# Kernel tuning notes

Measured on AMD Instinct MI355X. Metric: run time of the kernel, lower is better.

Reference implementation:

```python
import jax, jax.numpy as jnp
import numpy as np

B, G, K, KD = 16384, 17, 12, 16      # batch, games, kicks/game, kick feature dim
DK, DM, H, T = 16, 32, 2, 4          # d_kick, d_model, n_attn_heads, n_targets
SD, H1, H2, HH = 64, 256, 128, 32    # static_dim, backbone hidden dims, head hidden
AO = H * DM                          # attention output dim = 64
EPS = 1e-5
NEG_INF = float('-inf')


def setup_inputs() -> dict:
    ks = jax.random.split(jax.random.key(0), 18)
    n = lambda i, s, sc=0.05: jax.random.normal(ks[i], s, jnp.float32) * sc
    x_static = jax.random.normal(ks[0], (B, SD), jnp.float32)
    x_kicks = jax.random.normal(ks[1], (B, G, K, KD), jnp.float32)
    # masks: True = real game / kick; force position 0 valid so no row is fully padded
    outer_mask = jax.random.bernoulli(ks[2], 0.9, (B, G)).at[:, 0].set(True)
    inner_mask = jax.random.bernoulli(ks[3], 0.85, (B, G, K)).at[:, :, 0].set(True)
    return dict(
        x_static=x_static, x_kicks=x_kicks,
        W_ke=n(4, (KD, DK)), b_ke=jnp.zeros((DK,), jnp.float32),
        q_inner=n(5, (1, DK), 0.02),
        W_ge=n(6, (DK, DM)), b_ge=jnp.zeros((DM,), jnp.float32),
        pos_emb=n(7, (G, DM), 0.02),
        q_outer=n(8, (T * H, DM), 0.02),
        log_temp=jnp.zeros((T,), jnp.float32),
        ln_g=jnp.ones((T, AO), jnp.float32), ln_b=jnp.zeros((T, AO), jnp.float32),
        W1=n(9, (SD, H1)), b1=jnp.zeros((H1,), jnp.float32),
        g1=jnp.ones((H1,), jnp.float32), be1=jnp.zeros((H1,), jnp.float32),
        m1=n(10, (H1,)), v1=jax.random.uniform(ks[11], (H1,), jnp.float32) + 0.5,
        W2=n(12, (H1, H2)), b2=jnp.zeros((H2,), jnp.float32),
        g2=jnp.ones((H2,), jnp.float32), be2=jnp.zeros((H2,), jnp.float32),
        m2=n(13, (H2,)), v2=jax.random.uniform(ks[14], (H2,), jnp.float32) + 0.5,
        Wh1=n(15, (T, H2 + AO, HH)), bh1=jnp.zeros((T, HH), jnp.float32),
        Wh2=n(16, (T, HH)), bh2=jnp.zeros((T,), jnp.float32),
        outer_mask=outer_mask, inner_mask=inner_mask)


def _forward(x_static, x_kicks, W_ke, b_ke, q_inner, W_ge, b_ge, pos_emb,
             q_outer, log_temp, ln_g, ln_b, W1, b1, g1, be1, m1, v1,
             W2, b2, g2, be2, m2, v2, Wh1, bh1, Wh2, bh2,
             outer_mask, inner_mask):
    # kick encoder: Linear -> ReLU, [B,G,K,KD] -> [B,G,K,DK]
    kick_enc = jax.nn.relu(jnp.einsum('bgkd,de->bgke', x_kicks, W_ke) + b_ke)
    # inner AttentionPool: single learned query over kicks within each game
    ai = jnp.einsum('d,bgkd->bgk', q_inner[0], kick_enc) * (DK ** -0.5)
    ai = jnp.where(inner_mask, ai, NEG_INF)
    wi = jnp.nan_to_num(jax.nn.softmax(ai, axis=-1))       # all-masked rows -> 0
    per_game = jnp.einsum('bgk,bgkd->bgd', wi, kick_enc)   # [B,G,DK]
    # game encoder + learned positional embedding
    encoded = jax.nn.relu(per_game @ W_ge + b_ge) + pos_emb[None]  # [B,G,DM]
    # outer AttentionPool: T*H learned queries over games, per-target temperature
    ao = jnp.einsum('qd,bgd->bqg', q_outer, encoded) * (DM ** -0.5)
    ao = ao * jnp.repeat(jnp.exp(-log_temp), H)[None, :, None]
    ao = jnp.where(outer_mask[:, None, :], ao, NEG_INF)
    wo = jnp.nan_to_num(jax.nn.softmax(ao, axis=-1))
    pooled = jnp.einsum('bqg,bgd->bqd', wo, encoded).reshape(-1, T, AO)  # [B,T,64]
    # per-target LayerNorm on history vector
    mu = pooled.mean(-1, keepdims=True)
    var = ((pooled - mu) ** 2).mean(-1, keepdims=True)
    hist = (pooled - mu) * jax.lax.rsqrt(var + EPS) * ln_g[None] + ln_b[None]
    # backbone: Linear -> BatchNorm(eval) -> ReLU, x2 (dropout = identity in eval)
    z = jax.nn.relu((x_static @ W1 + b1 - m1) * jax.lax.rsqrt(v1 + EPS) * g1 + be1)
    z = jax.nn.relu((z @ W2 + b2 - m2) * jax.lax.rsqrt(v2 + EPS) * g2 + be2)
    # per-target heads on [shared_static ; history_vec]
    head_in = jnp.concatenate(
        [jnp.broadcast_to(z[:, None, :], (z.shape[0], T, H2)), hist], axis=-1)  # [B,T,192]
    h = jax.nn.relu(jnp.einsum('btd,tdh->bth', head_in, Wh1) + bh1[None])
    out = jnp.einsum('bth,th->bt', h, Wh2) + bh2[None]
    return jnp.maximum(out, 0.0)  # all targets non-negative (clamp, not softplus)


def reference(x_static, x_kicks, W_ke, b_ke, q_inner, W_ge, b_ge, pos_emb,
              q_outer, log_temp, ln_g, ln_b, W1, b1, g1, be1, m1, v1,
              W2, b2, g2, be2, m2, v2, Wh1, bh1, Wh2, bh2,
              outer_mask, inner_mask):
    return _forward(x_static, x_kicks, W_ke, b_ke, q_inner, W_ge, b_ge, pos_emb,
                    q_outer, log_temp, ln_g, ln_b, W1, b1, g1, be1, m1, v1,
                    W2, b2, g2, be2, m2, v2, Wh1, bh1, Wh2, bh2,
                    outer_mask, inner_mask)
```

## Files before the change

### kernel.cpp

```cpp
#include <hip/hip_runtime.h>
#include <math.h>

#define NEGM (-1e30f)

__device__ __forceinline__ float4 ld4(const float* p) { return *(const float4*)p; }
__device__ __forceinline__ void fma4(float4& a, float s, const float4 w) {
    a.x += s * w.x; a.y += s * w.y; a.z += s * w.z; a.w += s * w.w;
}
__device__ __forceinline__ float dot4(const float4 a, const float4 b) {
    return (a.x * b.x + a.y * b.y) + (a.z * b.z + a.w * b.w);
}
__device__ __forceinline__ void upd4(float4& p, float rm, float rw, const float4 a) {
    p.x = p.x * rm + rw * a.x; p.y = p.y * rm + rw * a.y;
    p.z = p.z * rm + rw * a.z; p.w = p.w * rm + rw * a.w;
}

__global__ __launch_bounds__(256) void hist_kernel(
    const float* __restrict__ x_kicks,
    const float* __restrict__ W_ke, const float* __restrict__ b_ke,
    const float* __restrict__ q_inner,
    const float* __restrict__ W_ge, const float* __restrict__ b_ge,
    const float* __restrict__ pos_emb, const float* __restrict__ q_outer,
    const float* __restrict__ log_temp,
    const float* __restrict__ ln_g, const float* __restrict__ ln_b,
    const int* __restrict__ outer_mask, const int* __restrict__ inner_mask,
    float* __restrict__ hist)
{
    __shared__ float s_wke[256];
    __shared__ float s_wge[512];
    __shared__ float s_qout[256];
    __shared__ float s_pg[4][17 * 20];
    __shared__ float s_enc[4][17 * 36];
    __shared__ float s_ao[4][136];

    const int tid  = threadIdx.x;
    const int wid  = tid >> 6;
    const int lane = tid & 63;
    const int b    = blockIdx.x * 4 + wid;

    s_wke[tid] = W_ke[tid];
    s_qout[tid] = q_outer[tid];
    s_wge[tid] = W_ge[tid];
    s_wge[tid + 256] = W_ge[tid + 256];
    __syncthreads();

    float* pg  = s_pg[wid];
    float* enc = s_enc[wid];
    float* ao  = s_ao[wid];

    if (lane < 51) {
        const float* xb = x_kicks + ((size_t)b * 204 + lane * 4) * 16;
        const int4 msk = *(const int4*)(inner_mask + (size_t)b * 204 + lane * 4);

        const float4 qi0 = ld4(q_inner + 0), qi1 = ld4(q_inner + 4);
        const float4 qi2 = ld4(q_inner + 8), qi3 = ld4(q_inner + 12);
        const float4 bk0 = ld4(b_ke + 0), bk1 = ld4(b_ke + 4);
        const float4 bk2 = ld4(b_ke + 8), bk3 = ld4(b_ke + 12);

        float m = NEGM, s = 0.f;
        float4 p0 = {0,0,0,0}, p1 = p0, p2 = p0, p3 = p0;

        #pragma unroll
        for (int pp = 0; pp < 4; ++pp) {
            float xs[16];
            {
                float4 x0 = ld4(xb + pp * 16 + 0), x1 = ld4(xb + pp * 16 + 4);
                float4 x2 = ld4(xb + pp * 16 + 8), x3 = ld4(xb + pp * 16 + 12);
                xs[0]=x0.x; xs[1]=x0.y; xs[2]=x0.z; xs[3]=x0.w;
                xs[4]=x1.x; xs[5]=x1.y; xs[6]=x1.z; xs[7]=x1.w;
                xs[8]=x2.x; xs[9]=x2.y; xs[10]=x2.z; xs[11]=x2.w;
                xs[12]=x3.x; xs[13]=x3.y; xs[14]=x3.z; xs[15]=x3.w;
            }
            float4 a0 = bk0, a1 = bk1, a2 = bk2, a3 = bk3;
            #pragma unroll
            for (int i = 0; i < 16; ++i) {
                float xi = xs[i];
                fma4(a0, xi, *(float4*)&s_wke[i * 16 + 0]);
                fma4(a1, xi, *(float4*)&s_wke[i * 16 + 4]);
                fma4(a2, xi, *(float4*)&s_wke[i * 16 + 8]);
                fma4(a3, xi, *(float4*)&s_wke[i * 16 + 12]);
            }
            a0.x=fmaxf(a0.x,0.f); a0.y=fmaxf(a0.y,0.f); a0.z=fmaxf(a0.z,0.f); a0.w=fmaxf(a0.w,0.f);
            a1.x=fmaxf(a1.x,0.f); a1.y=fmaxf(a1.y,0.f); a1.z=fmaxf(a1.z,0.f); a1.w=fmaxf(a1.w,0.f);
            a2.x=fmaxf(a2.x,0.f); a2.y=fmaxf(a2.y,0.f); a2.z=fmaxf(a2.z,0.f); a2.w=fmaxf(a2.w,0.f);
            a3.x=fmaxf(a3.x,0.f); a3.y=fmaxf(a3.y,0.f); a3.z=fmaxf(a3.z,0.f); a3.w=fmaxf(a3.w,0.f);

            float sc = (dot4(a0, qi0) + dot4(a1, qi1) + dot4(a2, qi2) + dot4(a3, qi3)) * 0.25f;
            int mk = (pp == 0) ? msk.x : (pp == 1) ? msk.y : (pp == 2) ? msk.z : msk.w;

            float scm = mk ? sc : NEGM;
            float mn = fmaxf(m, scm);
            float rm = __expf(m - mn);
            float rw = mk ? __expf(sc - mn) : 0.f;
            s = s * rm + rw;
            upd4(p0, rm, rw, a0); upd4(p1, rm, rw, a1);
            upd4(p2, rm, rw, a2); upd4(p3, rm, rw, a3);
            m = mn;
        }

        const int base = (lane / 3) * 3;
        float gm = fmaxf(fmaxf(__shfl(m, base), __shfl(m, base + 1)), __shfl(m, base + 2));
        float r  = __expf(m - gm);
        float sl = s * r;
        float gs = __shfl(sl, base) + __shfl(sl, base + 1) + __shfl(sl, base + 2);
        float c  = r / gs;
        p0.x*=c; p0.y*=c; p0.z*=c; p0.w*=c;
        p1.x*=c; p1.y*=c; p1.z*=c; p1.w*=c;
        p2.x*=c; p2.y*=c; p2.z*=c; p2.w*=c;
        p3.x*=c; p3.y*=c; p3.z*=c; p3.w*=c;

        float4 o0, o1, o2, o3;
        o0.x = __shfl(p0.x,base)+__shfl(p0.x,base+1)+__shfl(p0.x,base+2);
        o0.y = __shfl(p0.y,base)+__shfl(p0.y,base+1)+__shfl(p0.y,base+2);
        o0.z = __shfl(p0.z,base)+__shfl(p0.z,base+1)+__shfl(p0.z,base+2);
        o0.w = __shfl(p0.w,base)+__shfl(p0.w,base+1)+__shfl(p0.w,base+2);
        o1.x = __shfl(p1.x,base)+__shfl(p1.x,base+1)+__shfl(p1.x,base+2);
        o1.y = __shfl(p1.y,base)+__shfl(p1.y,base+1)+__shfl(p1.y,base+2);
        o1.z = __shfl(p1.z,base)+__shfl(p1.z,base+1)+__shfl(p1.z,base+2);
        o1.w = __shfl(p1.w,base)+__shfl(p1.w,base+1)+__shfl(p1.w,base+2);
        o2.x = __shfl(p2.x,base)+__shfl(p2.x,base+1)+__shfl(p2.x,base+2);
        o2.y = __shfl(p2.y,base)+__shfl(p2.y,base+1)+__shfl(p2.y,base+2);
        o2.z = __shfl(p2.z,base)+__shfl(p2.z,base+1)+__shfl(p2.z,base+2);
        o2.w = __shfl(p2.w,base)+__shfl(p2.w,base+1)+__shfl(p2.w,base+2);
        o3.x = __shfl(p3.x,base)+__shfl(p3.x,base+1)+__shfl(p3.x,base+2);
        o3.y = __shfl(p3.y,base)+__shfl(p3.y,base+1)+__shfl(p3.y,base+2);
        o3.z = __shfl(p3.z,base)+__shfl(p3.z,base+1)+__shfl(p3.z,base+2);
        o3.w = __shfl(p3.w,base)+__shfl(p3.w,base+1)+__shfl(p3.w,base+2);
        if (lane == base) {
            const int g = lane / 3;
            *(float4*)&pg[g * 20 + 0]  = o0;
            *(float4*)&pg[g * 20 + 4]  = o1;
            *(float4*)&pg[g * 20 + 8]  = o2;
            *(float4*)&pg[g * 20 + 12] = o3;
        }
    }
    __syncthreads();

    for (int t = lane; t < 136; t += 64) {
        const int g = t >> 3, dq = t & 7;
        float4 acc = ld4(b_ge + dq * 4);
        #pragma unroll
        for (int i = 0; i < 16; ++i) {
            float pv = pg[g * 20 + i];
            fma4(acc, pv, *(float4*)&s_wge[i * 32 + dq * 4]);
        }
        float4 pe = ld4(pos_emb + g * 32 + dq * 4);
        acc.x = fmaxf(acc.x, 0.f) + pe.x; acc.y = fmaxf(acc.y, 0.f) + pe.y;
        acc.z = fmaxf(acc.z, 0.f) + pe.z; acc.w = fmaxf(acc.w, 0.f) + pe.w;
        *(float4*)&enc[g * 36 + dq * 4] = acc;
    }
    __syncthreads();

    for (int t = lane; t < 136; t += 64) {
        const int q = t / 17, g = t - q * 17;
        float4 acc = {0.f, 0.f, 0.f, 0.f};
        #pragma unroll
        for (int i4 = 0; i4 < 8; ++i4) {
            float4 ev = *(float4*)&enc[g * 36 + i4 * 4];
            float4 qv = *(float4*)&s_qout[q * 32 + i4 * 4];
            acc.x += ev.x * qv.x; acc.y += ev.y * qv.y;
            acc.z += ev.z * qv.z; acc.w += ev.w * qv.w;
        }
        float s = (acc.x + acc.y) + (acc.z + acc.w);
        s *= 0.17677669529663687f * __expf(-log_temp[q >> 1]);
        ao[t] = outer_mask[b * 17 + g] ? s : NEGM;
    }
    __syncthreads();

    {
        const int q = lane >> 3, j = lane & 7;
        float s0 = ao[q * 17 + j];
        float s1 = ao[q * 17 + j + 8];
        float s2 = (j == 0) ? ao[q * 17 + 16] : NEGM;
        float m = fmaxf(fmaxf(s0, s1), s2);
        m = fmaxf(m, __shfl_xor(m, 1));
        m = fmaxf(m, __shfl_xor(m, 2));
        m = fmaxf(m, __shfl_xor(m, 4));
        float e0 = __expf(s0 - m), e1 = __expf(s1 - m);
        float e2 = (j == 0) ? __expf(s2 - m) : 0.f;
        float ssum = e0 + e1 + e2;
        ssum += __shfl_xor(ssum, 1);
        ssum += __shfl_xor(ssum, 2);
        ssum += __shfl_xor(ssum, 4);
        float inv = 1.f / ssum;
        ao[q * 17 + j] = e0 * inv;
        ao[q * 17 + j + 8] = e1 * inv;
        if (j == 0) ao[q * 17 + 16] = e2 * inv;
    }
    __syncthreads();

    {
        const int q = lane >> 3, dq = lane & 7;
        float4 acc = {0.f, 0.f, 0.f, 0.f};
        #pragma unroll
        for (int g = 0; g < 17; ++g) {
            float w = ao[q * 17 + g];
            fma4(acc, w, *(float4*)&enc[g * 36 + dq * 4]);
        }
        float s = (acc.x + acc.y) + (acc.z + acc.w);
        s += __shfl_xor(s, 1); s += __shfl_xor(s, 2);
        s += __shfl_xor(s, 4); s += __shfl_xor(s, 8);
        float mu = s * 0.015625f;
        float4 d;
        d.x = acc.x - mu; d.y = acc.y - mu; d.z = acc.z - mu; d.w = acc.w - mu;
        float v = (d.x * d.x + d.y * d.y) + (d.z * d.z + d.w * d.w);
        v += __shfl_xor(v, 1); v += __shfl_xor(v, 2);
        v += __shfl_xor(v, 4); v += __shfl_xor(v, 8);
        float rs = rsqrtf(v * 0.015625f + 1e-5f);
        float4 gam = ld4(ln_g + lane * 4);
        float4 bet = ld4(ln_b + lane * 4);
        float4 res;
        res.x = d.x * rs * gam.x + bet.x; res.y = d.y * rs * gam.y + bet.y;
        res.z = d.z * rs * gam.z + bet.z; res.w = d.w * rs * gam.w + bet.w;
        *(float4*)&hist[(size_t)b * 256 + lane * 4] = res;
    }
}

__global__ __launch_bounds__(256) void backbone_kernel(
    const float* __restrict__ x_static,
    const float* __restrict__ W1, const float* __restrict__ b1,
    const float* __restrict__ g1, const float* __restrict__ be1,
    const float* __restrict__ m1, const float* __restrict__ v1,
    const float* __restrict__ W2, const float* __restrict__ b2,
    const float* __restrict__ g2, const float* __restrict__ be2,
    const float* __restrict__ m2, const float* __restrict__ v2,
    const float* __restrict__ Wh1, const float* __restrict__ bh1,
    const float* __restrict__ Wh2, const float* __restrict__ bh2,
    const float* __restrict__ hist, float* __restrict__ out)
{
    __shared__ float s_x[16 * 64];
    __shared__ float s_z1[16 * 256];
    __shared__ float s_z2[16 * 132];

    const int tid = threadIdx.x;
    const int row0 = blockIdx.x * 16;

    for (int i = tid; i < 16 * 64; i += 256) s_x[i] = x_static[(size_t)row0 * 64 + i];
    __syncthreads();

    {
        const int col = tid;
        float acc[16];
        #pragma unroll
        for (int r = 0; r < 16; ++r) acc[r] = 0.f;
        for (int k = 0; k < 64; ++k) {
            float w = W1[k * 256 + col];
            #pragma unroll
            for (int r = 0; r < 16; ++r) acc[r] += s_x[r * 64 + k] * w;
        }
        float sc = rsqrtf(v1[col] + 1e-5f) * g1[col];
        float off = b1[col] - m1[col];
        float bb = be1[col];
        #pragma unroll
        for (int r = 0; r < 16; ++r)
            s_z1[r * 256 + col] = fmaxf((acc[r] + off) * sc + bb, 0.f);
    }
    __syncthreads();

    {
        const int col = tid & 127;
        const int r0 = (tid >> 7) * 8;
        float acc[8];
        #pragma unroll
        for (int r = 0; r < 8; ++r) acc[r] = 0.f;
        for (int k = 0; k < 256; ++k) {
            float w = W2[k * 128 + col];
            #pragma unroll
            for (int r = 0; r < 8; ++r) acc[r] += s_z1[(r0 + r) * 256 + k] * w;
        }
        float sc = rsqrtf(v2[col] + 1e-5f) * g2[col];
        float off = b2[col] - m2[col];
        float bb = be2[col];
        #pragma unroll
        for (int r = 0; r < 8; ++r)
            s_z2[(r0 + r) * 132 + col] = fmaxf((acc[r] + off) * sc + bb, 0.f);
    }
    __syncthreads();

    {
        const int p = tid >> 2;
        const int gl = tid & 3;
        const int row = p >> 2;
        const int tgt = p & 3;
        const int j0 = gl * 8;

        float acc[8];
        #pragma unroll
        for (int j = 0; j < 8; ++j) acc[j] = bh1[tgt * 32 + j0 + j];

        const float* w1p = Wh1 + (size_t)tgt * 192 * 32 + j0;
        for (int d = 0; d < 128; ++d) {
            float v = s_z2[row * 132 + d];
            float4 a = ld4(w1p + d * 32);
            float4 c = ld4(w1p + d * 32 + 4);
            acc[0] += v * a.x; acc[1] += v * a.y; acc[2] += v * a.z; acc[3] += v * a.w;
            acc[4] += v * c.x; acc[5] += v * c.y; acc[6] += v * c.z; acc[7] += v * c.w;
        }
        const float* hp = hist + (size_t)(row0 + row) * 256 + tgt * 64;
        const float* w1q = w1p + 128 * 32;
        for (int d = 0; d < 64; ++d) {
            float v = hp[d];
            float4 a = ld4(w1q + d * 32);
            float4 c = ld4(w1q + d * 32 + 4);
            acc[0] += v * a.x; acc[1] += v * a.y; acc[2] += v * a.z; acc[3] += v * a.w;
            acc[4] += v * c.x; acc[5] += v * c.y; acc[6] += v * c.z; acc[7] += v * c.w;
        }
        float ps = 0.f;
        #pragma unroll
        for (int j = 0; j < 8; ++j) ps += fmaxf(acc[j], 0.f) * Wh2[tgt * 32 + j0 + j];
        ps += __shfl_xor(ps, 1);
        ps += __shfl_xor(ps, 2);
        if (gl == 0) out[(size_t)(row0 + row) * 4 + tgt] = fmaxf(ps + bh2[tgt], 0.f);
    }
}

extern "C" void kernel_launch(void* const* d_in, const int* in_sizes, int n_in,
                              void* d_out, int out_size, void* d_ws, size_t ws_size,
                              hipStream_t stream) {
    const float* x_static = (const float*)d_in[0];
    const float* x_kicks  = (const float*)d_in[1];
    const float* W_ke     = (const float*)d_in[2];
    const float* b_ke     = (const float*)d_in[3];
    const float* q_inner  = (const float*)d_in[4];
    const float* W_ge     = (const float*)d_in[5];
    const float* b_ge     = (const float*)d_in[6];
    const float* pos_emb  = (const float*)d_in[7];
    const float* q_outer  = (const float*)d_in[8];
    const float* log_temp = (const float*)d_in[9];
    const float* ln_g     = (const float*)d_in[10];
    const float* ln_b     = (const float*)d_in[11];
    const float* W1       = (const float*)d_in[12];
    const float* b1       = (const float*)d_in[13];
    const float* g1       = (const float*)d_in[14];
    const float* be1      = (const float*)d_in[15];
    const float* m1       = (const float*)d_in[16];
    const float* v1       = (const float*)d_in[17];
    const float* W2       = (const float*)d_in[18];
    const float* b2       = (const float*)d_in[19];
    const float* g2       = (const float*)d_in[20];
    const float* be2      = (const float*)d_in[21];
    const float* m2       = (const float*)d_in[22];
    const float* v2       = (const float*)d_in[23];
    const float* Wh1      = (const float*)d_in[24];
    const float* bh1      = (const float*)d_in[25];
    const float* Wh2      = (const float*)d_in[26];
    const float* bh2      = (const float*)d_in[27];
    const int* outer_mask = (const int*)d_in[28];
    const int* inner_mask = (const int*)d_in[29];

    float* hist = (float*)d_ws;
    float* out  = (float*)d_out;

    hist_kernel<<<16384 / 4, 256, 0, stream>>>(
        x_kicks, W_ke, b_ke, q_inner, W_ge, b_ge, pos_emb, q_outer,
        log_temp, ln_g, ln_b, outer_mask, inner_mask, hist);

    backbone_kernel<<<16384 / 16, 256, 0, stream>>>(
        x_static, W1, b1, g1, be1, m1, v1, W2, b2, g2, be2, m2, v2,
        Wh1, bh1, Wh2, bh2, hist, out);
}
```

Measured before the change: 159.0 us.

## Fuse history attention and backbone MLP into one kernel via shared memory

```diff
diff --git a/kernel.cpp b/kernel.cpp
--- a/kernel.cpp
+++ b/kernel.cpp
@@ -2,6 +2,8 @@
 #include <math.h>
 
 #define NEGM (-1e30f)
+
+typedef float v2f __attribute__((ext_vector_type(2)));
 
 __device__ __forceinline__ float4 ld4(const float* p) { return *(const float4*)p; }
 __device__ __forceinline__ void fma4(float4& a, float s, const float4 w) {
@@ -15,7 +17,8 @@
     p.z = p.z * rm + rw * a.z; p.w = p.w * rm + rw * a.w;
 }
 
-__global__ __launch_bounds__(256) void hist_kernel(
+__global__ __launch_bounds__(512) void fused_kernel(
+    const float* __restrict__ x_static,
     const float* __restrict__ x_kicks,
     const float* __restrict__ W_ke, const float* __restrict__ b_ke,
     const float* __restrict__ q_inner,
@@ -23,30 +26,36 @@
     const float* __restrict__ pos_emb, const float* __restrict__ q_outer,
     const float* __restrict__ log_temp,
     const float* __restrict__ ln_g, const float* __restrict__ ln_b,
+    const float* __restrict__ W1, const float* __restrict__ b1,
+    const float* __restrict__ g1, const float* __restrict__ be1,
+    const float* __restrict__ m1, const float* __restrict__ v1,
+    const float* __restrict__ W2, const float* __restrict__ b2,
+    const float* __restrict__ g2, const float* __restrict__ be2,
+    const float* __restrict__ m2, const float* __restrict__ v2,
+    const float* __restrict__ Wh1, const float* __restrict__ bh1,
+    const float* __restrict__ Wh2, const float* __restrict__ bh2,
     const int* __restrict__ outer_mask, const int* __restrict__ inner_mask,
-    float* __restrict__ hist)
+    float* __restrict__ out)
 {
     __shared__ float s_wke[256];
     __shared__ float s_wge[512];
     __shared__ float s_qout[256];
-    __shared__ float s_pg[4][17 * 20];
-    __shared__ float s_enc[4][17 * 36];
-    __shared__ float s_ao[4][136];
+    __shared__ float s_hist[2048];
+    __shared__ float s_scr[8704];
 
     const int tid  = threadIdx.x;
     const int wid  = tid >> 6;
     const int lane = tid & 63;
-    const int b    = blockIdx.x * 4 + wid;
-
-    s_wke[tid] = W_ke[tid];
-    s_qout[tid] = q_outer[tid];
-    s_wge[tid] = W_ge[tid];
-    s_wge[tid + 256] = W_ge[tid + 256];
-    __syncthreads();
-
-    float* pg  = s_pg[wid];
-    float* enc = s_enc[wid];
-    float* ao  = s_ao[wid];
+    const int row0 = blockIdx.x * 8;
+    const int b    = row0 + wid;
+
+    if (tid < 256) { s_wke[tid] = W_ke[tid]; s_qout[tid] = q_outer[tid]; }
+    else { int t = tid - 256; s_wge[t] = W_ge[t]; s_wge[t + 256] = W_ge[t + 256]; }
+    __syncthreads();
+
+    float* pg  = s_scr + wid * 1088;
+    float* enc = pg + 340;
+    float* ao  = enc + 612;
 
     if (lane < 51) {
         const float* xb = x_kicks + ((size_t)b * 204 + lane * 4) * 16;
@@ -161,9 +170,9 @@
             acc.x += ev.x * qv.x; acc.y += ev.y * qv.y;
             acc.z += ev.z * qv.z; acc.w += ev.w * qv.w;
         }
-        float s = (acc.x + acc.y) + (acc.z + acc.w);
-        s *= 0.17677669529663687f * __expf(-log_temp[q >> 1]);
-        ao[t] = outer_mask[b * 17 + g] ? s : NEGM;
+        float sv = (acc.x + acc.y) + (acc.z + acc.w);
+        sv *= 0.17677669529663687f * __expf(-log_temp[q >> 1]);
+        ao[t] = outer_mask[b * 17 + g] ? sv : NEGM;
     }
     __syncthreads();
 
@@ -172,12 +181,12 @@
         float s0 = ao[q * 17 + j];
         float s1 = ao[q * 17 + j + 8];
         float s2 = (j == 0) ? ao[q * 17 + 16] : NEGM;
-        float m = fmaxf(fmaxf(s0, s1), s2);
-        m = fmaxf(m, __shfl_xor(m, 1));
-        m = fmaxf(m, __shfl_xor(m, 2));
-        m = fmaxf(m, __shfl_xor(m, 4));
-        float e0 = __expf(s0 - m), e1 = __expf(s1 - m);
-        float e2 = (j == 0) ? __expf(s2 - m) : 0.f;
+        float mx = fmaxf(fmaxf(s0, s1), s2);
+        mx = fmaxf(mx, __shfl_xor(mx, 1));
+        mx = fmaxf(mx, __shfl_xor(mx, 2));
+        mx = fmaxf(mx, __shfl_xor(mx, 4));
+        float e0 = __expf(s0 - mx), e1 = __expf(s1 - mx);
+        float e2 = (j == 0) ? __expf(s2 - mx) : 0.f;
         float ssum = e0 + e1 + e2;
         ssum += __shfl_xor(ssum, 1);
         ssum += __shfl_xor(ssum, 2);
@@ -197,10 +206,10 @@
             float w = ao[q * 17 + g];
             fma4(acc, w, *(float4*)&enc[g * 36 + dq * 4]);
         }
-        float s = (acc.x + acc.y) + (acc.z + acc.w);
-        s += __shfl_xor(s, 1); s += __shfl_xor(s, 2);
-        s += __shfl_xor(s, 4); s += __shfl_xor(s, 8);
-        float mu = s * 0.015625f;
+        float sv = (acc.x + acc.y) + (acc.z + acc.w);
+        sv += __shfl_xor(sv, 1); sv += __shfl_xor(sv, 2);
+        sv += __shfl_xor(sv, 4); sv += __shfl_xor(sv, 8);
+        float mu = sv * 0.015625f;
         float4 d;
         d.x = acc.x - mu; d.y = acc.y - mu; d.z = acc.z - mu; d.w = acc.w - mu;
         float v = (d.x * d.x + d.y * d.y) + (d.z * d.z + d.w * d.w);
@@ -212,104 +221,96 @@
         float4 res;
         res.x = d.x * rs * gam.x + bet.x; res.y = d.y * rs * gam.y + bet.y;
         res.z = d.z * rs * gam.z + bet.z; res.w = d.w * rs * gam.w + bet.w;
-        *(float4*)&hist[(size_t)b * 256 + lane * 4] = res;
-    }
-}
-
-__global__ __launch_bounds__(256) void backbone_kernel(
-    const float* __restrict__ x_static,
-    const float* __restrict__ W1, const float* __restrict__ b1,
-    const float* __restrict__ g1, const float* __restrict__ be1,
-    const float* __restrict__ m1, const float* __restrict__ v1,
-    const float* __restrict__ W2, const float* __restrict__ b2,
-    const float* __restrict__ g2, const float* __restrict__ be2,
-    const float* __restrict__ m2, const float* __restrict__ v2,
-    const float* __restrict__ Wh1, const float* __restrict__ bh1,
-    const float* __restrict__ Wh2, const float* __restrict__ bh2,
-    const float* __restrict__ hist, float* __restrict__ out)
-{
-    __shared__ float s_x[16 * 64];
-    __shared__ float s_z1[16 * 256];
-    __shared__ float s_z2[16 * 132];
-
-    const int tid = threadIdx.x;
-    const int row0 = blockIdx.x * 16;
-
-    for (int i = tid; i < 16 * 64; i += 256) s_x[i] = x_static[(size_t)row0 * 64 + i];
-    __syncthreads();
-
-    {
-        const int col = tid;
-        float acc[16];
-        #pragma unroll
-        for (int r = 0; r < 16; ++r) acc[r] = 0.f;
-        for (int k = 0; k < 64; ++k) {
-            float w = W1[k * 256 + col];
+        *(float4*)&s_hist[wid * 256 + lane * 4] = res;
+    }
+    __syncthreads();
+
+    float* s_x  = s_scr;
+    float* s_z1 = s_scr + 512;
+    float* s_z2 = s_scr + 2560;
+
+    s_x[tid] = x_static[(size_t)row0 * 64 + tid];
+    __syncthreads();
+
+    {
+        const int col = tid & 255;
+        const int r0 = (tid >> 8) * 4;
+        float acc[4] = {0.f, 0.f, 0.f, 0.f};
+        for (int k4 = 0; k4 < 16; ++k4) {
+            float w0 = W1[(k4 * 4 + 0) * 256 + col];
+            float w1 = W1[(k4 * 4 + 1) * 256 + col];
+            float w2 = W1[(k4 * 4 + 2) * 256 + col];
+            float w3 = W1[(k4 * 4 + 3) * 256 + col];
             #pragma unroll
-            for (int r = 0; r < 16; ++r) acc[r] += s_x[r * 64 + k] * w;
+            for (int r = 0; r < 4; ++r) {
+                float4 xv = *(float4*)&s_x[(r0 + r) * 64 + k4 * 4];
+                acc[r] += xv.x * w0 + xv.y * w1 + xv.z * w2 + xv.w * w3;
+            }
         }
         float sc = rsqrtf(v1[col] + 1e-5f) * g1[col];
         float off = b1[col] - m1[col];
         float bb = be1[col];
         #pragma unroll
-        for (int r = 0; r < 16; ++r)
-            s_z1[r * 256 + col] = fmaxf((acc[r] + off) * sc + bb, 0.f);
+        for (int r = 0; r < 4; ++r)
+            s_z1[(r0 + r) * 256 + col] = fmaxf((acc[r] + off) * sc + bb, 0.f);
     }
     __syncthreads();
 
     {
         const int col = tid & 127;
-        const int r0 = (tid >> 7) * 8;
-        float acc[8];
-        #pragma unroll
-        for (int r = 0; r < 8; ++r) acc[r] = 0.f;
-        for (int k = 0; k < 256; ++k) {
-            float w = W2[k * 128 + col];
+        const int r0 = (tid >> 7) * 2;
+        float acc[2] = {0.f, 0.f};
+        for (int k4 = 0; k4 < 64; ++k4) {
+            float w0 = W2[(k4 * 4 + 0) * 128 + col];
+            float w1 = W2[(k4 * 4 + 1) * 128 + col];
+            float w2 = W2[(k4 * 4 + 2) * 128 + col];
+            float w3 = W2[(k4 * 4 + 3) * 128 + col];
             #pragma unroll
-            for (int r = 0; r < 8; ++r) acc[r] += s_z1[(r0 + r) * 256 + k] * w;
+            for (int r = 0; r < 2; ++r) {
+                float4 zv = *(float4*)&s_z1[(r0 + r) * 256 + k4 * 4];
+                acc[r] += zv.x * w0 + zv.y * w1 + zv.z * w2 + zv.w * w3;
+            }
         }
         float sc = rsqrtf(v2[col] + 1e-5f) * g2[col];
         float off = b2[col] - m2[col];
         float bb = be2[col];
         #pragma unroll
-        for (int r = 0; r < 8; ++r)
+        for (int r = 0; r < 2; ++r)
             s_z2[(r0 + r) * 132 + col] = fmaxf((acc[r] + off) * sc + bb, 0.f);
     }
     __syncthreads();
 
     {
-        const int p = tid >> 2;
-        const int gl = tid & 3;
+        const int p = tid >> 4;
+        const int gl = tid & 15;
         const int row = p >> 2;
         const int tgt = p & 3;
-        const int j0 = gl * 8;
-
-        float acc[8];
-        #pragma unroll
-        for (int j = 0; j < 8; ++j) acc[j] = bh1[tgt * 32 + j0 + j];
-
+        const int j0 = gl * 2;
+
+        v2f acc = *(const v2f*)(bh1 + tgt * 32 + j0);
         const float* w1p = Wh1 + (size_t)tgt * 192 * 32 + j0;
-        for (int d = 0; d < 128; ++d) {
-            float v = s_z2[row * 132 + d];
-            float4 a = ld4(w1p + d * 32);
-            float4 c = ld4(w1p + d * 32 + 4);
-            acc[0] += v * a.x; acc[1] += v * a.y; acc[2] += v * a.z; acc[3] += v * a.w;
-            acc[4] += v * c.x; acc[5] += v * c.y; acc[6] += v * c.z; acc[7] += v * c.w;
-        }
-        const float* hp = hist + (size_t)(row0 + row) * 256 + tgt * 64;
+        for (int d4 = 0; d4 < 32; ++d4) {
+            float4 zv = *(float4*)&s_z2[row * 132 + d4 * 4];
+            acc += v2f{zv.x, zv.x} * *(const v2f*)(w1p + (d4 * 4 + 0) * 32);
+            acc += v2f{zv.y, zv.y} * *(const v2f*)(w1p + (d4 * 4 + 1) * 32);
+            acc += v2f{zv.z, zv.z} * *(const v2f*)(w1p + (d4 * 4 + 2) * 32);
+            acc += v2f{zv.w, zv.w} * *(const v2f*)(w1p + (d4 * 4 + 3) * 32);
+        }
+        const float* hp = s_hist + row * 256 + tgt * 64;
         const float* w1q = w1p + 128 * 32;
-        for (int d = 0; d < 64; ++d) {
-            float v = hp[d];
-            float4 a = ld4(w1q + d * 32);
-            float4 c = ld4(w1q + d * 32 + 4);
-            acc[0] += v * a.x; acc[1] += v * a.y; acc[2] += v * a.z; acc[3] += v * a.w;
-            acc[4] += v * c.x; acc[5] += v * c.y; acc[6] += v * c.z; acc[7] += v * c.w;
-        }
-        float ps = 0.f;
-        #pragma unroll
-        for (int j = 0; j < 8; ++j) ps += fmaxf(acc[j], 0.f) * Wh2[tgt * 32 + j0 + j];
+        for (int d4 = 0; d4 < 16; ++d4) {
+            float4 hv = *(float4*)&hp[d4 * 4];
+            acc += v2f{hv.x, hv.x} * *(const v2f*)(w1q + (d4 * 4 + 0) * 32);
+            acc += v2f{hv.y, hv.y} * *(const v2f*)(w1q + (d4 * 4 + 1) * 32);
+            acc += v2f{hv.z, hv.z} * *(const v2f*)(w1q + (d4 * 4 + 2) * 32);
+            acc += v2f{hv.w, hv.w} * *(const v2f*)(w1q + (d4 * 4 + 3) * 32);
+        }
+        float ps = fmaxf(acc.x, 0.f) * Wh2[tgt * 32 + j0]
+                 + fmaxf(acc.y, 0.f) * Wh2[tgt * 32 + j0 + 1];
         ps += __shfl_xor(ps, 1);
         ps += __shfl_xor(ps, 2);
+        ps += __shfl_xor(ps, 4);
+        ps += __shfl_xor(ps, 8);
         if (gl == 0) out[(size_t)(row0 + row) * 4 + tgt] = fmaxf(ps + bh2[tgt], 0.f);
     }
 }
@@ -348,14 +349,11 @@
     const int* outer_mask = (const int*)d_in[28];
     const int* inner_mask = (const int*)d_in[29];
 
-    float* hist = (float*)d_ws;
-    float* out  = (float*)d_out;
-
-    hist_kernel<<<16384 / 4, 256, 0, stream>>>(
-        x_kicks, W_ke, b_ke, q_inner, W_ge, b_ge, pos_emb, q_outer,
-        log_temp, ln_g, ln_b, outer_mask, inner_mask, hist);
-
-    backbone_kernel<<<16384 / 16, 256, 0, stream>>>(
-        x_static, W1, b1, g1, be1, m1, v1, W2, b2, g2, be2, m2, v2,
-        Wh1, bh1, Wh2, bh2, hist, out);
-}
+    float* out = (float*)d_out;
+
+    fused_kernel<<<16384 / 8, 512, 0, stream>>>(
+        x_static, x_kicks, W_ke, b_ke, q_inner, W_ge, b_ge, pos_emb, q_outer,
+        log_temp, ln_g, ln_b, W1, b1, g1, be1, m1, v1,
+        W2, b2, g2, be2, m2, v2, Wh1, bh1, Wh2, bh2,
+        outer_mask, inner_mask, out);
+}
```

New measurement: 254.9 us. 1.6x slower.
